# Optimization experiments

Hardware: AMD Instinct MI355X
Metric: run time of the kernel (lower is better)

Reference implementation:

```python
import jax, jax.numpy as jnp
import numpy as np

N, IN_DIM, H, D = 4096, 512, 8, 64
NEG = -1e9  # additive mask value for non-edges


def setup_inputs() -> dict:
    key = jax.random.key(0)
    k1, k2, k3, k4, k5, k6 = jax.random.split(key, 6)
    data = jax.random.normal(k1, (N, IN_DIM), dtype=jnp.float32)
    r = jax.random.uniform(k2, (N, N), dtype=jnp.float32)
    connectivity = jnp.where(r < 0.05, 0.0, NEG).astype(jnp.float32)
    # xavier-uniform-ish init for params
    lim_w = float(np.sqrt(6.0 / (IN_DIM + H * D)))
    W = jax.random.uniform(k3, (H * D, IN_DIM), jnp.float32, -lim_w, lim_w)
    b = jnp.zeros((H * D,), jnp.float32)
    lim_p = float(np.sqrt(6.0 / (H * D + 1)))
    src_proj = jax.random.uniform(k4, (1, H, D), jnp.float32, -lim_p, lim_p)
    trg_proj = jax.random.uniform(k5, (1, H, D), jnp.float32, -lim_p, lim_p)
    return {"data": data, "connectivity": connectivity, "W": W, "b": b,
            "src_proj": src_proj, "trg_proj": trg_proj}


def reference(data, connectivity, W, b, src_proj, trg_proj):
    # dropout is identity in eval mode (reference is deterministic)
    data1 = (data @ W.T + b).reshape(N, H, D)          # (N,H,D)
    src = jnp.einsum('nhd,xhd->nh', data1, src_proj)   # (N,H)
    trg = jnp.einsum('nhd,xhd->nh', data1, trg_proj)   # (N,H)
    # scores: (H,N,1) + (H,1,N) broadcast outer-sum
    e = src.T[:, :, None] + trg.T[:, None, :]          # (H,N,N)
    e = jnp.where(e >= 0, e, 0.01 * e)                 # LeakyReLU(0.01)
    e = e + connectivity[None, :, :]                   # additive mask
    scores = jax.nn.softmax(e, axis=-1)                # (H,N,N)
    # bmm over heads: (H,N,N) x (H,N,D) -> (H,N,D)
    out = jnp.einsum('hnm,hmd->hnd', scores, data1.transpose(1, 0, 2))
    out = out.transpose(1, 0, 2).reshape(N, H * D)     # concat=True
    return out
```

## Files before the change

### kernel.cpp

```cpp
#include <hip/hip_runtime.h>
#include <hip/hip_bf16.h>

#define NN 4096
#define IN_DIM 512
#define NH 8
#define DD 64
#define HD 512
#define QCAP 128


typedef __attribute__((ext_vector_type(8))) short short8;
typedef __attribute__((ext_vector_type(4))) float f32x4;

static __device__ __forceinline__ unsigned short f2bf(float x) {
    __hip_bfloat16 h = __float2bfloat16(x);
    return *reinterpret_cast<unsigned short*>(&h);
}

__global__ __launch_bounds__(256) void k_cast2(const float* __restrict__ inA,
                                               unsigned short* __restrict__ outA,
                                               int n4A,
                                               const float* __restrict__ inB,
                                               unsigned short* __restrict__ outB,
                                               int n4B) {
    int t = blockIdx.x * 256 + threadIdx.x;
    const float* in;
    unsigned short* out;
    if (t < n4A) {
        in = inA; out = outA;
    } else {
        t -= n4A;
        if (t >= n4B) return;
        in = inB; out = outB;
    }
    float4 v = ((const float4*)in)[t];
    ushort4 o;
    o.x = f2bf(v.x); o.y = f2bf(v.y); o.z = f2bf(v.z); o.w = f2bf(v.w);
    ((ushort4*)out)[t] = o;
}

__global__ __launch_bounds__(256) void k_gemm_fused(const unsigned short* __restrict__ Ab,
                                                    const unsigned short* __restrict__ Wb,
                                                    const float* __restrict__ bias,
                                                    const float* __restrict__ sp,
                                                    const float* __restrict__ tp,
                                                    unsigned short* __restrict__ Cb,
                                                    float* __restrict__ src,
                                                    float* __restrict__ trg) {
    const int lane = threadIdx.x & 63;
    const int w = threadIdx.x >> 6;
    const int col = lane & 15;
    const int quad = lane >> 4;
    const int koff = quad * 8;
    const int h = blockIdx.x;
    const int m0 = h * 64;
    const int n0 = blockIdx.y * 64;

    const short8* ap  = (const short8*)(Ab + (size_t)(n0 + w * 16 + col) * IN_DIM + koff);
    const short8* bp0 = (const short8*)(Wb + (size_t)(m0 +  0 + col) * IN_DIM + koff);
    const short8* bp1 = (const short8*)(Wb + (size_t)(m0 + 16 + col) * IN_DIM + koff);
    const short8* bp2 = (const short8*)(Wb + (size_t)(m0 + 32 + col) * IN_DIM + koff);
    const short8* bp3 = (const short8*)(Wb + (size_t)(m0 + 48 + col) * IN_DIM + koff);

    f32x4 acc0 = {0.f, 0.f, 0.f, 0.f}, acc1 = acc0, acc2 = acc0, acc3 = acc0;

#pragma unroll 4
    for (int ks = 0; ks < 16; ks++) {
        short8 a  = ap[ks * 4];
        short8 b0 = bp0[ks * 4];
        short8 b1 = bp1[ks * 4];
        short8 b2 = bp2[ks * 4];
        short8 b3 = bp3[ks * 4];
        acc0 = __builtin_amdgcn_mfma_f32_16x16x32_bf16(a, b0, acc0, 0, 0, 0);
        acc1 = __builtin_amdgcn_mfma_f32_16x16x32_bf16(a, b1, acc1, 0, 0, 0);
        acc2 = __builtin_amdgcn_mfma_f32_16x16x32_bf16(a, b2, acc2, 0, 0, 0);
        acc3 = __builtin_amdgcn_mfma_f32_16x16x32_bf16(a, b3, acc3, 0, 0, 0);
    }

    const int rbase = n0 + w * 16 + quad * 4;
    f32x4 accs[4] = {acc0, acc1, acc2, acc3};
    float ps[4] = {0.f, 0.f, 0.f, 0.f};
    float pt[4] = {0.f, 0.f, 0.f, 0.f};
#pragma unroll
    for (int mt = 0; mt < 4; mt++) {
        const int m = m0 + mt * 16 + col;
        const float bv  = bias[m];
        const float spv = sp[m];
        const float tpv = tp[m];
#pragma unroll
        for (int r = 0; r < 4; r++) {
            float v = accs[mt][r] + bv;
            Cb[(size_t)(rbase + r) * HD + m] = f2bf(v);
            ps[r] += v * spv;
            pt[r] += v * tpv;
        }
    }
#pragma unroll
    for (int off = 1; off <= 8; off <<= 1) {
#pragma unroll
        for (int r = 0; r < 4; r++) {
            ps[r] += __shfl_xor(ps[r], off, 64);
            pt[r] += __shfl_xor(pt[r], off, 64);
        }
    }
    if (col < 4)
        src[(rbase + col) * 8 + h] = ps[col];
    else if (col < 8)
        trg[(rbase + col - 4) * 8 + h] = pt[col - 4];
}

__global__ __launch_bounds__(256) void k_rowattn(const float* __restrict__ conn,
                                                 const float* __restrict__ src,
                                                 const float* __restrict__ trg,
                                                 const unsigned short* __restrict__ d1b,
                                                 float* __restrict__ out) {
    __shared__ unsigned short ebuf[4][QCAP];
    __shared__ float cbuf[3][64][9];
    const int w = threadIdx.x >> 6, lane = threadIdx.x & 63;
    const int i = blockIdx.x;
    const int h = lane >> 3, d8 = lane & 7;

    const float* crow = conn + (size_t)i * NN + w * 1024;
    int cnt = 0;
#pragma unroll
    for (int c0 = 0; c0 < 1024; c0 += 256) {
        float4 c = *(const float4*)(crow + c0 + lane * 4);
        float cv[4] = {c.x, c.y, c.z, c.w};
#pragma unroll
        for (int q = 0; q < 4; q++) {
            bool edge = (cv[q] == 0.0f);
            unsigned long long mask = __ballot(edge);
            int pre = __popcll(mask & ((1ull << lane) - 1ull));
            int pos = cnt + pre;
            if (edge && pos < QCAP)
                ebuf[w][pos] = (unsigned short)(w * 1024 + c0 + lane * 4 + q);
            cnt += __popcll(mask);
        }
    }
    if (cnt > QCAP) cnt = QCAP;
    __syncthreads();

    const float sh = src[i * 8 + h];
    const unsigned voffB = (unsigned)(h * 64 + d8 * 8) * 2u;
    const unsigned toffB = (unsigned)h << 2;
    const unsigned char* vb = (const unsigned char*)d1b;
    const unsigned char* tb = (const unsigned char*)trg;

    float acc[8] = {0.f, 0.f, 0.f, 0.f, 0.f, 0.f, 0.f, 0.f};
    float lsum = 0.f;
    if (cnt > 0) {
        const int cm1 = cnt - 1;
        unsigned j0 = ebuf[w][0];
        unsigned j1 = ebuf[w][(1 <= cm1) ? 1 : cm1];
        unsigned j2 = ebuf[w][(2 <= cm1) ? 2 : cm1];
        float t0 = *(const float*)(tb + (j0 << 5) + toffB);
        float t1 = *(const float*)(tb + (j1 << 5) + toffB);
        uint4 U0 = *(const uint4*)(vb + (j0 << 10) + voffB);
        uint4 U1 = *(const uint4*)(vb + (j1 << 10) + voffB);
#pragma unroll 3
        for (int k = 0; k < cnt; k++) {
            unsigned j3 = ebuf[w][(k + 3 <= cm1) ? (k + 3) : cm1];
            float t2 = *(const float*)(tb + (j2 << 5) + toffB);
            uint4 U2 = *(const uint4*)(vb + (j2 << 10) + voffB);
            float e = sh + t0;
            e = fmaxf(e, 0.01f * e);
            float p = __expf(e);
            lsum += p;
            acc[0] += p * __uint_as_float(U0.x << 16);
            acc[1] += p * __uint_as_float(U0.x & 0xffff0000u);
            acc[2] += p * __uint_as_float(U0.y << 16);
            acc[3] += p * __uint_as_float(U0.y & 0xffff0000u);
            acc[4] += p * __uint_as_float(U0.z << 16);
            acc[5] += p * __uint_as_float(U0.z & 0xffff0000u);
            acc[6] += p * __uint_as_float(U0.w << 16);
            acc[7] += p * __uint_as_float(U0.w & 0xffff0000u);
            t0 = t1; t1 = t2;
            U0 = U1; U1 = U2;
            j2 = j3;
        }
    }

    if (w > 0) {
#pragma unroll
        for (int r = 0; r < 8; r++) cbuf[w - 1][lane][r] = acc[r];
        cbuf[w - 1][lane][8] = lsum;
    }
    __syncthreads();
    if (w == 0) {
#pragma unroll
        for (int wv = 0; wv < 3; wv++) {
#pragma unroll
            for (int r = 0; r < 8; r++) acc[r] += cbuf[wv][lane][r];
            lsum += cbuf[wv][lane][8];
        }
        float inv = (lsum > 0.f) ? (1.f / lsum) : 0.f;
        float* op = out + (size_t)i * HD + h * 64 + d8 * 8;
        *(float4*)op = make_float4(acc[0] * inv, acc[1] * inv, acc[2] * inv, acc[3] * inv);
        *(float4*)(op + 4) = make_float4(acc[4] * inv, acc[5] * inv, acc[6] * inv, acc[7] * inv);
    }
}

extern "C" void kernel_launch(void* const* d_in, const int* in_sizes, int n_in,
                              void* d_out, int out_size, void* d_ws, size_t ws_size,
                              hipStream_t stream) {
    const float* data = (const float*)d_in[0];
    const float* conn = (const float*)d_in[1];
    const float* W    = (const float*)d_in[2];
    const float* bias = (const float*)d_in[3];
    const float* sp   = (const float*)d_in[4];
    const float* tp   = (const float*)d_in[5];
    float* out = (float*)d_out;

    unsigned short* d1b = (unsigned short*)d_ws;
    unsigned short* Ab  = d1b + (size_t)NN * HD;
    unsigned short* Wb  = Ab + (size_t)NN * IN_DIM;
    float* src  = (float*)(Wb + (size_t)HD * IN_DIM);
    float* trg  = src + NN * NH;

    const int n4A = NN * IN_DIM / 4;
    const int n4B = HD * IN_DIM / 4;
    k_cast2<<<dim3((n4A + n4B + 255) / 256), 256, 0, stream>>>(data, Ab, n4A, W, Wb, n4B);
    k_gemm_fused<<<dim3(NH, NN / 64), 256, 0, stream>>>(Ab, Wb, bias, sp, tp, d1b, src, trg);
    k_rowattn<<<dim3(NN), 256, 0, stream>>>(conn, src, trg, d1b, out);
}
```

Baseline: 169.6 us.

## Fuse bf16 cast into GEMM and rebalance edge lists across waves

Drops the separate fp32-to-bf16 cast kernel. The GEMM now loads fp32 data and W directly and converts them in registers, which saves one launch and a full write and re-read of the bf16 copies. It also redoes the attention kernel: the per-wave edge segments are merged into one shared list, split evenly across the four waves, and padded so the prefetch needs no clamping. This evens out the work between waves. The cost is an extra synchronisation and twice the global bytes per GEMM operand load, since W is re-read as fp32 by every row block.

Measured after the change: 185.3 us. 1.09x slower.

```diff
diff --git a/kernel.cpp b/kernel.cpp
--- a/kernel.cpp
+++ b/kernel.cpp
@@ -7,6 +7,7 @@
 #define DD 64
 #define HD 512
 #define QCAP 128
+#define RCAP 448
 
 
 typedef __attribute__((ext_vector_type(8))) short short8;
@@ -17,36 +18,23 @@
     return *reinterpret_cast<unsigned short*>(&h);
 }
 
-__global__ __launch_bounds__(256) void k_cast2(const float* __restrict__ inA,
-                                               unsigned short* __restrict__ outA,
-                                               int n4A,
-                                               const float* __restrict__ inB,
-                                               unsigned short* __restrict__ outB,
-                                               int n4B) {
-    int t = blockIdx.x * 256 + threadIdx.x;
-    const float* in;
-    unsigned short* out;
-    if (t < n4A) {
-        in = inA; out = outA;
-    } else {
-        t -= n4A;
-        if (t >= n4B) return;
-        in = inB; out = outB;
-    }
-    float4 v = ((const float4*)in)[t];
-    ushort4 o;
-    o.x = f2bf(v.x); o.y = f2bf(v.y); o.z = f2bf(v.z); o.w = f2bf(v.w);
-    ((ushort4*)out)[t] = o;
-}
-
-__global__ __launch_bounds__(256) void k_gemm_fused(const unsigned short* __restrict__ Ab,
-                                                    const unsigned short* __restrict__ Wb,
-                                                    const float* __restrict__ bias,
-                                                    const float* __restrict__ sp,
-                                                    const float* __restrict__ tp,
-                                                    unsigned short* __restrict__ Cb,
-                                                    float* __restrict__ src,
-                                                    float* __restrict__ trg) {
+static __device__ __forceinline__ short8 cvt8(float4 a, float4 b) {
+    short8 r;
+    r[0] = (short)f2bf(a.x); r[1] = (short)f2bf(a.y);
+    r[2] = (short)f2bf(a.z); r[3] = (short)f2bf(a.w);
+    r[4] = (short)f2bf(b.x); r[5] = (short)f2bf(b.y);
+    r[6] = (short)f2bf(b.z); r[7] = (short)f2bf(b.w);
+    return r;
+}
+
+__global__ __launch_bounds__(256) void k_prep(const float* __restrict__ A,
+                                              const float* __restrict__ W,
+                                              const float* __restrict__ bias,
+                                              const float* __restrict__ sp,
+                                              const float* __restrict__ tp,
+                                              unsigned short* __restrict__ Cb,
+                                              float* __restrict__ src,
+                                              float* __restrict__ trg) {
     const int lane = threadIdx.x & 63;
     const int w = threadIdx.x >> 6;
     const int col = lane & 15;
@@ -56,21 +44,22 @@
     const int m0 = h * 64;
     const int n0 = blockIdx.y * 64;
 
-    const short8* ap  = (const short8*)(Ab + (size_t)(n0 + w * 16 + col) * IN_DIM + koff);
-    const short8* bp0 = (const short8*)(Wb + (size_t)(m0 +  0 + col) * IN_DIM + koff);
-    const short8* bp1 = (const short8*)(Wb + (size_t)(m0 + 16 + col) * IN_DIM + koff);
-    const short8* bp2 = (const short8*)(Wb + (size_t)(m0 + 32 + col) * IN_DIM + koff);
-    const short8* bp3 = (const short8*)(Wb + (size_t)(m0 + 48 + col) * IN_DIM + koff);
+    const float* apf  = A + (size_t)(n0 + w * 16 + col) * IN_DIM + koff;
+    const float* bpf0 = W + (size_t)(m0 +  0 + col) * IN_DIM + koff;
+    const float* bpf1 = W + (size_t)(m0 + 16 + col) * IN_DIM + koff;
+    const float* bpf2 = W + (size_t)(m0 + 32 + col) * IN_DIM + koff;
+    const float* bpf3 = W + (size_t)(m0 + 48 + col) * IN_DIM + koff;
 
     f32x4 acc0 = {0.f, 0.f, 0.f, 0.f}, acc1 = acc0, acc2 = acc0, acc3 = acc0;
 
 #pragma unroll 4
     for (int ks = 0; ks < 16; ks++) {
-        short8 a  = ap[ks * 4];
-        short8 b0 = bp0[ks * 4];
-        short8 b1 = bp1[ks * 4];
-        short8 b2 = bp2[ks * 4];
-        short8 b3 = bp3[ks * 4];
+        const int o = ks * 32;
+        short8 a  = cvt8(*(const float4*)(apf  + o), *(const float4*)(apf  + o + 4));
+        short8 b0 = cvt8(*(const float4*)(bpf0 + o), *(const float4*)(bpf0 + o + 4));
+        short8 b1 = cvt8(*(const float4*)(bpf1 + o), *(const float4*)(bpf1 + o + 4));
+        short8 b2 = cvt8(*(const float4*)(bpf2 + o), *(const float4*)(bpf2 + o + 4));
+        short8 b3 = cvt8(*(const float4*)(bpf3 + o), *(const float4*)(bpf3 + o + 4));
         acc0 = __builtin_amdgcn_mfma_f32_16x16x32_bf16(a, b0, acc0, 0, 0, 0);
         acc1 = __builtin_amdgcn_mfma_f32_16x16x32_bf16(a, b1, acc1, 0, 0, 0);
         acc2 = __builtin_amdgcn_mfma_f32_16x16x32_bf16(a, b2, acc2, 0, 0, 0);
@@ -114,7 +103,9 @@
                                                  const float* __restrict__ trg,
                                                  const unsigned short* __restrict__ d1b,
                                                  float* __restrict__ out) {
-    __shared__ unsigned short ebuf[4][QCAP];
+    __shared__ unsigned short seg[4][QCAP];
+    __shared__ unsigned short elist[RCAP + 8];
+    __shared__ int wcnt[4];
     __shared__ float cbuf[3][64][9];
     const int w = threadIdx.x >> 6, lane = threadIdx.x & 63;
     const int i = blockIdx.x;
@@ -133,11 +124,24 @@
             int pre = __popcll(mask & ((1ull << lane) - 1ull));
             int pos = cnt + pre;
             if (edge && pos < QCAP)
-                ebuf[w][pos] = (unsigned short)(w * 1024 + c0 + lane * 4 + q);
+                seg[w][pos] = (unsigned short)(w * 1024 + c0 + lane * 4 + q);
             cnt += __popcll(mask);
         }
     }
     if (cnt > QCAP) cnt = QCAP;
+    if (lane == 0) wcnt[w] = cnt;
+    __syncthreads();
+
+    const int c0n = wcnt[0], c1n = wcnt[1], c2n = wcnt[2], c3n = wcnt[3];
+    int tot = c0n + c1n + c2n + c3n;
+    if (tot > RCAP) tot = RCAP;
+    const int base = (w == 0) ? 0 : (w == 1) ? c0n
+                   : (w == 2) ? c0n + c1n : c0n + c1n + c2n;
+    for (int k = lane; k < cnt && base + k < RCAP; k += 64)
+        elist[base + k] = seg[w][k];
+    __syncthreads();
+    if (threadIdx.x < 4)
+        elist[tot + threadIdx.x] = (tot > 0) ? elist[tot - 1] : (unsigned short)0;
     __syncthreads();
 
     const float sh = src[i * 8 + h];
@@ -145,21 +149,22 @@
     const unsigned toffB = (unsigned)h << 2;
     const unsigned char* vb = (const unsigned char*)d1b;
     const unsigned char* tb = (const unsigned char*)trg;
+    const int kbeg = (tot * w) >> 2;
+    const int kend = (tot * (w + 1)) >> 2;
 
     float acc[8] = {0.f, 0.f, 0.f, 0.f, 0.f, 0.f, 0.f, 0.f};
     float lsum = 0.f;
-    if (cnt > 0) {
-        const int cm1 = cnt - 1;
-        unsigned j0 = ebuf[w][0];
-        unsigned j1 = ebuf[w][(1 <= cm1) ? 1 : cm1];
-        unsigned j2 = ebuf[w][(2 <= cm1) ? 2 : cm1];
+    if (kend > kbeg) {
+        unsigned j0 = elist[kbeg];
+        unsigned j1 = elist[kbeg + 1];
+        unsigned j2 = elist[kbeg + 2];
         float t0 = *(const float*)(tb + (j0 << 5) + toffB);
         float t1 = *(const float*)(tb + (j1 << 5) + toffB);
         uint4 U0 = *(const uint4*)(vb + (j0 << 10) + voffB);
         uint4 U1 = *(const uint4*)(vb + (j1 << 10) + voffB);
 #pragma unroll 3
-        for (int k = 0; k < cnt; k++) {
-            unsigned j3 = ebuf[w][(k + 3 <= cm1) ? (k + 3) : cm1];
+        for (int k = kbeg; k < kend; k++) {
+            unsigned j3 = elist[k + 3];
             float t2 = *(const float*)(tb + (j2 << 5) + toffB);
             uint4 U2 = *(const uint4*)(vb + (j2 << 10) + voffB);
             float e = sh + t0;
@@ -212,14 +217,9 @@
     float* out = (float*)d_out;
 
     unsigned short* d1b = (unsigned short*)d_ws;
-    unsigned short* Ab  = d1b + (size_t)NN * HD;
-    unsigned short* Wb  = Ab + (size_t)NN * IN_DIM;
-    float* src  = (float*)(Wb + (size_t)HD * IN_DIM);
+    float* src  = (float*)(d1b + (size_t)NN * HD);
     float* trg  = src + NN * NH;
 
-    const int n4A = NN * IN_DIM / 4;
-    const int n4B = HD * IN_DIM / 4;
-    k_cast2<<<dim3((n4A + n4B + 255) / 256), 256, 0, stream>>>(data, Ab, n4A, W, Wb, n4B);
-    k_gemm_fused<<<dim3(NH, NN / 64), 256, 0, stream>>>(Ab, Wb, bias, sp, tp, d1b, src, trg);
+    k_prep<<<dim3(NH, NN / 64), 256, 0, stream>>>(data, W, bias, sp, tp, d1b, src, trg);
     k_rowattn<<<dim3(NN), 256, 0, stream>>>(conn, src, trg, d1b, out);
 }
```

## Balance edge work across waves via compacted edge list and packed FMA

Applied to the files above, without the earlier changes.

Each wave's edges from its quarter of the row are gathered into a single compacted shared-memory list, and that list is split evenly among the four waves. Before, each wave processed only the edges in its own column segment, so the load could be uneven. The accumulation also moves to two-wide float vectors so the compiler can emit packed FMA instructions. This adds an extra block-wide sync and a copy step, and it caps the total at RCAP edges.

New measurement: 166.2 us. 2.0% less time.

```diff
diff --git a/kernel.cpp b/kernel.cpp
--- a/kernel.cpp
+++ b/kernel.cpp
@@ -7,10 +7,12 @@
 #define DD 64
 #define HD 512
 #define QCAP 128
+#define RCAP 448
 
 
 typedef __attribute__((ext_vector_type(8))) short short8;
 typedef __attribute__((ext_vector_type(4))) float f32x4;
+typedef __attribute__((ext_vector_type(2))) float f32x2;
 
 static __device__ __forceinline__ unsigned short f2bf(float x) {
     __hip_bfloat16 h = __float2bfloat16(x);
@@ -114,7 +116,9 @@
                                                  const float* __restrict__ trg,
                                                  const unsigned short* __restrict__ d1b,
                                                  float* __restrict__ out) {
-    __shared__ unsigned short ebuf[4][QCAP];
+    __shared__ unsigned short seg[4][QCAP];
+    __shared__ unsigned short elist[RCAP + 8];
+    __shared__ int wcnt[4];
     __shared__ float cbuf[3][64][9];
     const int w = threadIdx.x >> 6, lane = threadIdx.x & 63;
     const int i = blockIdx.x;
@@ -133,11 +137,24 @@
             int pre = __popcll(mask & ((1ull << lane) - 1ull));
             int pos = cnt + pre;
             if (edge && pos < QCAP)
-                ebuf[w][pos] = (unsigned short)(w * 1024 + c0 + lane * 4 + q);
+                seg[w][pos] = (unsigned short)(w * 1024 + c0 + lane * 4 + q);
             cnt += __popcll(mask);
         }
     }
     if (cnt > QCAP) cnt = QCAP;
+    if (lane == 0) wcnt[w] = cnt;
+    __syncthreads();
+
+    const int c0n = wcnt[0], c1n = wcnt[1], c2n = wcnt[2], c3n = wcnt[3];
+    int tot = c0n + c1n + c2n + c3n;
+    if (tot > RCAP) tot = RCAP;
+    const int base = (w == 0) ? 0 : (w == 1) ? c0n
+                   : (w == 2) ? c0n + c1n : c0n + c1n + c2n;
+    for (int k = lane; k < cnt && base + k < RCAP; k += 64)
+        elist[base + k] = seg[w][k];
+    __syncthreads();
+    if (threadIdx.x < 4)
+        elist[tot + threadIdx.x] = (tot > 0) ? elist[tot - 1] : (unsigned short)0;
     __syncthreads();
 
     const float sh = src[i * 8 + h];
@@ -145,41 +162,44 @@
     const unsigned toffB = (unsigned)h << 2;
     const unsigned char* vb = (const unsigned char*)d1b;
     const unsigned char* tb = (const unsigned char*)trg;
-
-    float acc[8] = {0.f, 0.f, 0.f, 0.f, 0.f, 0.f, 0.f, 0.f};
+    const int kbeg = (tot * w) >> 2;
+    const int kend = (tot * (w + 1)) >> 2;
+
+    f32x2 a01 = {0.f, 0.f}, a23 = a01, a45 = a01, a67 = a01;
     float lsum = 0.f;
-    if (cnt > 0) {
-        const int cm1 = cnt - 1;
-        unsigned j0 = ebuf[w][0];
-        unsigned j1 = ebuf[w][(1 <= cm1) ? 1 : cm1];
-        unsigned j2 = ebuf[w][(2 <= cm1) ? 2 : cm1];
+    if (kend > kbeg) {
+        unsigned j0 = elist[kbeg];
+        unsigned j1 = elist[kbeg + 1];
+        unsigned j2 = elist[kbeg + 2];
         float t0 = *(const float*)(tb + (j0 << 5) + toffB);
         float t1 = *(const float*)(tb + (j1 << 5) + toffB);
         uint4 U0 = *(const uint4*)(vb + (j0 << 10) + voffB);
         uint4 U1 = *(const uint4*)(vb + (j1 << 10) + voffB);
 #pragma unroll 3
-        for (int k = 0; k < cnt; k++) {
-            unsigned j3 = ebuf[w][(k + 3 <= cm1) ? (k + 3) : cm1];
+        for (int k = kbeg; k < kend; k++) {
+            unsigned j3 = elist[k + 3];
             float t2 = *(const float*)(tb + (j2 << 5) + toffB);
             uint4 U2 = *(const uint4*)(vb + (j2 << 10) + voffB);
             float e = sh + t0;
             e = fmaxf(e, 0.01f * e);
             float p = __expf(e);
             lsum += p;
-            acc[0] += p * __uint_as_float(U0.x << 16);
-            acc[1] += p * __uint_as_float(U0.x & 0xffff0000u);
-            acc[2] += p * __uint_as_float(U0.y << 16);
-            acc[3] += p * __uint_as_float(U0.y & 0xffff0000u);
-            acc[4] += p * __uint_as_float(U0.z << 16);
-            acc[5] += p * __uint_as_float(U0.z & 0xffff0000u);
-            acc[6] += p * __uint_as_float(U0.w << 16);
-            acc[7] += p * __uint_as_float(U0.w & 0xffff0000u);
+            f32x2 p2 = {p, p};
+            f32x2 v01 = {__uint_as_float(U0.x << 16), __uint_as_float(U0.x & 0xffff0000u)};
+            f32x2 v23 = {__uint_as_float(U0.y << 16), __uint_as_float(U0.y & 0xffff0000u)};
+            f32x2 v45 = {__uint_as_float(U0.z << 16), __uint_as_float(U0.z & 0xffff0000u)};
+            f32x2 v67 = {__uint_as_float(U0.w << 16), __uint_as_float(U0.w & 0xffff0000u)};
+            a01 += p2 * v01;
+            a23 += p2 * v23;
+            a45 += p2 * v45;
+            a67 += p2 * v67;
             t0 = t1; t1 = t2;
             U0 = U1; U1 = U2;
             j2 = j3;
         }
     }
 
+    float acc[8] = {a01.x, a01.y, a23.x, a23.y, a45.x, a45.y, a67.x, a67.y};
     if (w > 0) {
 #pragma unroll
         for (int r = 0; r < 8; r++) cbuf[w - 1][lane][r] = acc[r];
```
